# Kernel optimization log

Hardware: AMD Instinct MI355X
Metric: run time of the kernel (lower is better)

## Reference

```python
import jax, jax.numpy as jnp
import numpy as np

EPS = 1e-4

def safe_clamp(x, max_val):
    # nan -> 0, +inf -> max_val, -inf -> -max_val, then clamp to [-max_val, max_val]
    x = jnp.where(jnp.isnan(x), 0.0, x)
    x = jnp.where(jnp.isinf(x) & (x > 0), max_val, x)
    x = jnp.where(jnp.isinf(x) & (x < 0), -max_val, x)
    return jnp.clip(x, -max_val, max_val)

def setup_inputs() -> dict:
    key = jax.random.key(0)
    k1, k2 = jax.random.split(key)
    hidden_states = jax.random.normal(k1, (4, 4096, 2048), dtype=jnp.float32)
    ln_weight = jnp.ones((2048,), dtype=jnp.float32)
    ln_bias = jnp.zeros((2048,), dtype=jnp.float32)
    gate_weight = jax.random.normal(k2, (64, 2048), dtype=jnp.float32) * 0.01
    return {"hidden_states": hidden_states, "ln_weight": ln_weight,
            "ln_bias": ln_bias, "gate_weight": gate_weight}

def reference(hidden_states, ln_weight, ln_bias, gate_weight):
    B, S, H = hidden_states.shape
    top_k = 2
    x = hidden_states.reshape(-1, H)  # (N, H)
    # LayerNorm(eps=1e-5)
    mu = jnp.mean(x, axis=-1, keepdims=True)
    var = jnp.mean((x - mu) ** 2, axis=-1, keepdims=True)
    x = (x - mu) * jax.lax.rsqrt(var + 1e-5) * ln_weight + ln_bias
    x = safe_clamp(x, 50.0)
    # gate: (N, H) @ (H, E)
    router_logits = jnp.clip(x @ gate_weight.T, -10.0, 10.0)
    # eval mode: no noise
    router_probs = jnp.clip(jax.nn.softmax(router_logits, axis=-1), EPS, 1.0)
    top_k_probs, top_k_indices = jax.lax.top_k(router_probs, top_k)
    prob_sum = jnp.maximum(jnp.sum(top_k_probs, axis=-1, keepdims=True), EPS)
    top_k_probs = top_k_probs / prob_sum
    return top_k_probs, top_k_indices, router_logits
```

## Files before the change

kernel.cpp:

```cpp
#include <hip/hip_runtime.h>
#include <math.h>

#define H 2048
#define E 64
#define MR 16
#define NCH 16
#define LR 136

typedef _Float16 half8  __attribute__((ext_vector_type(8)));
typedef _Float16 half4h __attribute__((ext_vector_type(4)));
typedef float    f32x4  __attribute__((ext_vector_type(4)));

#define MFMA16(A,B,C) __builtin_amdgcn_mfma_f32_16x16x32_f16(A,B,C,0,0,0)


__global__ __launch_bounds__(256) void prep_fused(const float* __restrict__ W,
        const float* __restrict__ lnw, const float* __restrict__ lnb,
        _Float16* __restrict__ Bh, _Float16* __restrict__ Bl,
        float* __restrict__ csum, float* __restrict__ bsum) {
    {
        int idx  = blockIdx.x * 256 + threadIdx.x;
        int lane = idx & 63;
        int e  = ((idx >> 6) & 3) * 16 + (lane & 15);
        int k0 = (idx >> 8) * 32 + ((lane >> 4) << 3);
        half8 hh, ll;
        #pragma unroll
        for (int j = 0; j < 8; ++j) {
            float wf = lnw[k0 + j] * W[e * H + k0 + j];
            _Float16 h = (_Float16)wf;
            _Float16 l = (_Float16)((wf - (float)h) * 2048.0f);
            hh[j] = h; ll[j] = l;
        }
        *(half8*)&Bh[(long)idx * 8] = hh;
        *(half8*)&Bl[(long)idx * 8] = ll;
    }
    {
        __shared__ float rc[256], rb[256];
        int e = blockIdx.x, t = threadIdx.x;
        float cs = 0.f, bs = 0.f;
        #pragma unroll
        for (int j = 0; j < 8; ++j) {
            int k = t + j * 256;
            float w = W[e * H + k];
            cs += lnw[k] * w;
            bs += lnb[k] * w;
        }
        rc[t] = cs; rb[t] = bs;
        __syncthreads();
        for (int s = 128; s > 0; s >>= 1) {
            if (t < s) { rc[t] += rc[t + s]; rb[t] += rb[t + s]; }
            __syncthreads();
        }
        if (t == 0) { csum[e] = rc[0]; bsum[e] = rb[0]; }
    }
}

__global__ __launch_bounds__(256, 4) void router_kernel(
    const float* __restrict__ X, const _Float16* __restrict__ Bh,
    const _Float16* __restrict__ Bl, const float* __restrict__ csum,
    const float* __restrict__ bsum, float* __restrict__ out, int nRows)
{
    __shared__ __align__(16) _Float16 Xh[2][MR][LR];
    __shared__ __align__(16) _Float16 Xl[2][MR][LR];
    __shared__ float C2[MR][E + 4];
    __shared__ float mu_s[MR], rs_s[MR];

    const int t    = threadIdx.x;
    const int lane = t & 63;
    const int et   = t >> 6;
    const int q    = lane >> 4;
    const int ln16 = lane & 15;
    const int rowR = t >> 4;
    const int cS   = t & 15;
    const long rowBase = (long)blockIdx.x * MR;
    const long iOff = (long)nRows * 2;
    const long lOff = (long)nRows * 4;

    const float4* Xrow = (const float4*)X + (rowBase + rowR) * 512;

    float sacc = 0.f, qacc = 0.f;
    f32x4 acc0 = (f32x4)0.f;
    f32x4 acc1 = (f32x4)0.f;

    auto convert = [&](float4 v0_, float4 v1_, int buf) {
        #pragma unroll
        for (int j = 0; j < 2; ++j) {
            float4 v = j ? v1_ : v0_;
            sacc += v.x + v.y + v.z + v.w;
            qacc += v.x * v.x + v.y * v.y + v.z * v.z + v.w * v.w;
            _Float16 h0 = (_Float16)v.x, h1 = (_Float16)v.y,
                     h2 = (_Float16)v.z, h3 = (_Float16)v.w;
            _Float16 l0 = (_Float16)((v.x - (float)h0) * 2048.f);
            _Float16 l1 = (_Float16)((v.y - (float)h1) * 2048.f);
            _Float16 l2 = (_Float16)((v.z - (float)h2) * 2048.f);
            _Float16 l3 = (_Float16)((v.w - (float)h3) * 2048.f);
            half4h hh = {h0, h1, h2, h3};
            half4h ll = {l0, l1, l2, l3};
            int col = (cS + j * 16) * 4;
            *(half4h*)&Xh[buf][rowR][col] = hh;
            *(half4h*)&Xl[buf][rowR][col] = ll;
        }
    };
    auto loadW = [&](half8* Wh, half8* Wl, int c) {
        #pragma unroll
        for (int ks = 0; ks < 4; ++ks) {
            int bo = (((c * 4 + ks) * 4 + et) * 64 + lane) * 8;
            Wh[ks] = *(const half8*)&Bh[bo];
            Wl[ks] = *(const half8*)&Bl[bo];
        }
    };
    auto mfmaC = [&](const half8* Wh, const half8* Wl, int buf) {
        #pragma unroll
        for (int ks = 0; ks < 4; ++ks) {
            half8 Ah = *(const half8*)&Xh[buf][ln16][ks * 32 + q * 8];
            half8 Al = *(const half8*)&Xl[buf][ln16][ks * 32 + q * 8];
            acc0 = MFMA16(Ah, Wh[ks], acc0);
            acc1 = MFMA16(Ah, Wl[ks], acc1);
            acc1 = MFMA16(Al, Wh[ks], acc1);
        }
    };

    float4 vA0, vA1, vB0, vB1;

    {
        float4 v00 = Xrow[cS];
        float4 v01 = Xrow[cS + 16];
        vA0 = Xrow[32 + cS];
        vA1 = Xrow[32 + cS + 16];
        convert(v00, v01, 0);
    }
    __syncthreads();

    for (int c = 0; c < NCH; c += 2) {
        {
            half8 Wh[4], Wl[4];
            loadW(Wh, Wl, c);
            if (c + 2 < NCH) {
                vB0 = Xrow[(c + 2) * 32 + cS];
                vB1 = Xrow[(c + 2) * 32 + cS + 16];
            }
            mfmaC(Wh, Wl, 0);
            convert(vA0, vA1, 1);
        }
        __syncthreads();

        {
            half8 Wh[4], Wl[4];
            loadW(Wh, Wl, c + 1);
            if (c + 3 < NCH) {
                vA0 = Xrow[(c + 3) * 32 + cS];
                vA1 = Xrow[(c + 3) * 32 + cS + 16];
            }
            mfmaC(Wh, Wl, 1);
            if (c + 2 < NCH) convert(vB0, vB1, 0);
        }
        __syncthreads();
    }

    {
        float s = sacc, qq = qacc;
        #pragma unroll
        for (int d = 1; d < 16; d <<= 1) {
            s  += __shfl_xor(s, d);
            qq += __shfl_xor(qq, d);
        }
        if (cS == 0) {
            float mu  = s * (1.f / H);
            float var = qq * (1.f / H) - mu * mu;
            mu_s[rowR] = mu;
            rs_s[rowR] = rsqrtf(var + 1e-5f);
        }
    }
    __syncthreads();

    {
        int n = et * 16 + ln16;
        float cs = csum[n], bs = bsum[n];
        #pragma unroll
        for (int reg = 0; reg < 4; ++reg) {
            int r = q * 4 + reg;
            float raw = acc0[reg] + acc1[reg] * (1.f / 2048.f);
            float lg = rs_s[r] * (raw - mu_s[r] * cs) + bs;
            lg = fminf(fmaxf(lg, -10.f), 10.f);
            out[lOff + (rowBase + r) * 64 + n] = lg;
            C2[r][n] = lg;
        }
    }
    __syncthreads();

    #pragma unroll
    for (int rr = 0; rr < 4; ++rr) {
        int r = et * 4 + rr;
        float l = C2[r][lane];
        float m = l;
        #pragma unroll
        for (int d = 1; d < 64; d <<= 1) m = fmaxf(m, __shfl_xor(m, d));
        float p = __expf(l - m);
        float ssum = p;
        #pragma unroll
        for (int d = 1; d < 64; d <<= 1) ssum += __shfl_xor(ssum, d);
        float prob = fminf(fmaxf(p / ssum, 1e-4f), 1.0f);

        float v1 = prob; int i1 = lane;
        #pragma unroll
        for (int d = 1; d < 64; d <<= 1) {
            float ov = __shfl_xor(v1, d);
            int   oi = __shfl_xor(i1, d);
            if (ov > v1 || (ov == v1 && oi < i1)) { v1 = ov; i1 = oi; }
        }
        float v2 = (lane == i1) ? -1.f : prob; int i2 = lane;
        #pragma unroll
        for (int d = 1; d < 64; d <<= 1) {
            float ov = __shfl_xor(v2, d);
            int   oi = __shfl_xor(i2, d);
            if (ov > v2 || (ov == v2 && oi < i2)) { v2 = ov; i2 = oi; }
        }
        if (lane == 0) {
            float ps = fmaxf(v1 + v2, 1e-4f);
            long rg_ = rowBase + r;
            out[rg_ * 2 + 0] = v1 / ps;
            out[rg_ * 2 + 1] = v2 / ps;
            out[iOff + rg_ * 2 + 0] = (float)i1;
            out[iOff + rg_ * 2 + 1] = (float)i2;
        }
    }
}

extern "C" void kernel_launch(void* const* d_in, const int* in_sizes, int n_in,
                              void* d_out, int out_size, void* d_ws, size_t ws_size,
                              hipStream_t stream) {
    const float* X   = (const float*)d_in[0];
    const float* lnw = (const float*)d_in[1];
    const float* lnb = (const float*)d_in[2];
    const float* W   = (const float*)d_in[3];
    float* outp = (float*)d_out;

    _Float16* Bh = (_Float16*)d_ws;
    _Float16* Bl = Bh + H * E;
    float* csum  = (float*)(Bl + H * E);
    float* bsum  = csum + E;

    int N = in_sizes[0] / H;

    prep_fused<<<64, 256, 0, stream>>>(W, lnw, lnb, Bh, Bl, csum, bsum);
    router_kernel<<<N / MR, 256, 0, stream>>>(X, Bh, Bl, csum, bsum, outp, N);
}
```

Measured before the change: 214.6 us.

## Halve rows per block to eight with padded zero row for MFMA

Each block now processes 8 token rows instead of 16. The MFMA A tile is padded with a shared zero row so lanes 8-15 read zeros, and the unused half of the accumulator output is discarded. The change doubles the block count and raises the launch-bounds occupancy hint to 6, aiming for more memory-level parallelism on the bandwidth-bound X stream. In exchange it wastes half of the MFMA work and doubles the per-block reloads of the W tiles from global/L2.

```diff
diff --git a/kernel.cpp b/kernel.cpp
--- a/kernel.cpp
+++ b/kernel.cpp
@@ -3,7 +3,7 @@
 
 #define H 2048
 #define E 64
-#define MR 16
+#define MR 8
 #define NCH 16
 #define LR 136
 
@@ -55,13 +55,13 @@
     }
 }
 
-__global__ __launch_bounds__(256, 4) void router_kernel(
+__global__ __launch_bounds__(256, 6) void router_kernel(
     const float* __restrict__ X, const _Float16* __restrict__ Bh,
     const _Float16* __restrict__ Bl, const float* __restrict__ csum,
     const float* __restrict__ bsum, float* __restrict__ out, int nRows)
 {
-    __shared__ __align__(16) _Float16 Xh[2][MR][LR];
-    __shared__ __align__(16) _Float16 Xl[2][MR][LR];
+    __shared__ __align__(16) _Float16 Xh[2][MR + 1][LR];
+    __shared__ __align__(16) _Float16 Xl[2][MR + 1][LR];
     __shared__ float C2[MR][E + 4];
     __shared__ float mu_s[MR], rs_s[MR];
 
@@ -70,36 +70,37 @@
     const int et   = t >> 6;
     const int q    = lane >> 4;
     const int ln16 = lane & 15;
-    const int rowR = t >> 4;
-    const int cS   = t & 15;
+    const int arow = (ln16 < MR) ? ln16 : MR;
+    const int rowR = t >> 5;
+    const int cS   = t & 31;
     const long rowBase = (long)blockIdx.x * MR;
     const long iOff = (long)nRows * 2;
     const long lOff = (long)nRows * 4;
 
     const float4* Xrow = (const float4*)X + (rowBase + rowR) * 512;
 
+    if (t < LR) {
+        Xh[0][MR][t] = (_Float16)0.f; Xh[1][MR][t] = (_Float16)0.f;
+        Xl[0][MR][t] = (_Float16)0.f; Xl[1][MR][t] = (_Float16)0.f;
+    }
+
     float sacc = 0.f, qacc = 0.f;
     f32x4 acc0 = (f32x4)0.f;
     f32x4 acc1 = (f32x4)0.f;
 
-    auto convert = [&](float4 v0_, float4 v1_, int buf) {
-        #pragma unroll
-        for (int j = 0; j < 2; ++j) {
-            float4 v = j ? v1_ : v0_;
-            sacc += v.x + v.y + v.z + v.w;
-            qacc += v.x * v.x + v.y * v.y + v.z * v.z + v.w * v.w;
-            _Float16 h0 = (_Float16)v.x, h1 = (_Float16)v.y,
-                     h2 = (_Float16)v.z, h3 = (_Float16)v.w;
-            _Float16 l0 = (_Float16)((v.x - (float)h0) * 2048.f);
-            _Float16 l1 = (_Float16)((v.y - (float)h1) * 2048.f);
-            _Float16 l2 = (_Float16)((v.z - (float)h2) * 2048.f);
-            _Float16 l3 = (_Float16)((v.w - (float)h3) * 2048.f);
-            half4h hh = {h0, h1, h2, h3};
-            half4h ll = {l0, l1, l2, l3};
-            int col = (cS + j * 16) * 4;
-            *(half4h*)&Xh[buf][rowR][col] = hh;
-            *(half4h*)&Xl[buf][rowR][col] = ll;
-        }
+    auto convert = [&](float4 v, int buf) {
+        sacc += v.x + v.y + v.z + v.w;
+        qacc += v.x * v.x + v.y * v.y + v.z * v.z + v.w * v.w;
+        _Float16 h0 = (_Float16)v.x, h1 = (_Float16)v.y,
+                 h2 = (_Float16)v.z, h3 = (_Float16)v.w;
+        _Float16 l0 = (_Float16)((v.x - (float)h0) * 2048.f);
+        _Float16 l1 = (_Float16)((v.y - (float)h1) * 2048.f);
+        _Float16 l2 = (_Float16)((v.z - (float)h2) * 2048.f);
+        _Float16 l3 = (_Float16)((v.w - (float)h3) * 2048.f);
+        half4h hh = {h0, h1, h2, h3};
+        half4h ll = {l0, l1, l2, l3};
+        *(half4h*)&Xh[buf][rowR][cS * 4] = hh;
+        *(half4h*)&Xl[buf][rowR][cS * 4] = ll;
     };
     auto loadW = [&](half8* Wh, half8* Wl, int c) {
         #pragma unroll
@@ -112,22 +113,20 @@
     auto mfmaC = [&](const half8* Wh, const half8* Wl, int buf) {
         #pragma unroll
         for (int ks = 0; ks < 4; ++ks) {
-            half8 Ah = *(const half8*)&Xh[buf][ln16][ks * 32 + q * 8];
-            half8 Al = *(const half8*)&Xl[buf][ln16][ks * 32 + q * 8];
+            half8 Ah = *(const half8*)&Xh[buf][arow][ks * 32 + q * 8];
+            half8 Al = *(const half8*)&Xl[buf][arow][ks * 32 + q * 8];
             acc0 = MFMA16(Ah, Wh[ks], acc0);
             acc1 = MFMA16(Ah, Wl[ks], acc1);
             acc1 = MFMA16(Al, Wh[ks], acc1);
         }
     };
 
-    float4 vA0, vA1, vB0, vB1;
+    float4 vA0, vB0;
 
     {
         float4 v00 = Xrow[cS];
-        float4 v01 = Xrow[cS + 16];
         vA0 = Xrow[32 + cS];
-        vA1 = Xrow[32 + cS + 16];
-        convert(v00, v01, 0);
+        convert(v00, 0);
     }
     __syncthreads();
 
@@ -135,24 +134,18 @@
         {
             half8 Wh[4], Wl[4];
             loadW(Wh, Wl, c);
-            if (c + 2 < NCH) {
-                vB0 = Xrow[(c + 2) * 32 + cS];
-                vB1 = Xrow[(c + 2) * 32 + cS + 16];
-            }
+            if (c + 2 < NCH) vB0 = Xrow[(c + 2) * 32 + cS];
             mfmaC(Wh, Wl, 0);
-            convert(vA0, vA1, 1);
+            convert(vA0, 1);
         }
         __syncthreads();
 
         {
             half8 Wh[4], Wl[4];
             loadW(Wh, Wl, c + 1);
-            if (c + 3 < NCH) {
-                vA0 = Xrow[(c + 3) * 32 + cS];
-                vA1 = Xrow[(c + 3) * 32 + cS + 16];
-            }
+            if (c + 3 < NCH) vA0 = Xrow[(c + 3) * 32 + cS];
             mfmaC(Wh, Wl, 1);
-            if (c + 2 < NCH) convert(vB0, vB1, 0);
+            if (c + 2 < NCH) convert(vB0, 0);
         }
         __syncthreads();
     }
@@ -160,7 +153,7 @@
     {
         float s = sacc, qq = qacc;
         #pragma unroll
-        for (int d = 1; d < 16; d <<= 1) {
+        for (int d = 1; d < 32; d <<= 1) {
             s  += __shfl_xor(s, d);
             qq += __shfl_xor(qq, d);
         }
@@ -173,7 +166,7 @@
     }
     __syncthreads();
 
-    {
+    if (q < 2) {
         int n = et * 16 + ln16;
         float cs = csum[n], bs = bsum[n];
         #pragma unroll
@@ -189,8 +182,8 @@
     __syncthreads();
 
     #pragma unroll
-    for (int rr = 0; rr < 4; ++rr) {
-        int r = et * 4 + rr;
+    for (int rr = 0; rr < 2; ++rr) {
+        int r = et * 2 + rr;
         float l = C2[r][lane];
         float m = l;
         #pragma unroll
```

After: 289.0 us. 34.6% more time.
